# Kernel optimization log

Measured on AMD Instinct MI355X. Metric: run time of the kernel, lower is better.

Reference implementation:

```python
import jax, jax.numpy as jnp
import numpy as np

B, N, T, S = 32, 102400, 64, 1600
PI = float(np.pi)
EPS = 1e-12  # numerical guard inside sqrt for cdist (diagonal is exactly 0)


def _cdist(a, b):
    # a: (..., P, 3), b: (..., Q, 3) -> (..., P, Q) euclidean distances
    sq = jnp.sum((a[..., :, None, :] - b[..., None, :, :]) ** 2, axis=-1)
    return jnp.sqrt(sq + EPS)


def _rigid_t(alpha, trans, sz, center):
    # alpha, trans: (B, T, 3). Returns XYZ (B,T,3,3), translation (B,T,3).
    c, s = jnp.cos(alpha), jnp.sin(alpha)
    z = jnp.zeros_like(c[..., 0]); o = jnp.ones_like(c[..., 0])
    X = jnp.stack([c[..., 0], -s[..., 0], z, s[..., 0], c[..., 0], z, z, z, o], -1).reshape(*alpha.shape[:2], 3, 3)
    Y = jnp.stack([c[..., 1], z, s[..., 1], z, o, z, -s[..., 1], z, c[..., 1]], -1).reshape(*alpha.shape[:2], 3, 3)
    Z = jnp.stack([o, z, z, z, c[..., 2], -s[..., 2], z, s[..., 2], c[..., 2]], -1).reshape(*alpha.shape[:2], 3, 3)
    XYZ = jnp.einsum('btij,btjk,btkl->btil', X, Y, Z)
    eye = jnp.eye(3, dtype=alpha.dtype)
    Tt = trans * sz[None, None, :] + jnp.einsum('m,btmk->btk', center, eye[None, None] - XYZ)
    return XYZ, Tt


def setup_inputs():
    key = jax.random.key(0)
    ks = jax.random.split(key, 6)
    x = jax.random.normal(ks[0], (B, 6, N), jnp.float32)
    w1 = jax.random.normal(ks[1], (3 * N, 32), jnp.float32) * 0.005
    b1 = jnp.zeros((32,), jnp.float32)
    w2 = jax.random.normal(ks[2], (32, 6 * T), jnp.float32) * 0.05
    b2 = jnp.zeros((6 * T,), jnp.float32)
    A = jax.random.normal(ks[3], (6, N), jnp.float32)
    mask = jax.random.uniform(ks[4], (T, T), jnp.float32)
    sz = jnp.array([128.0, 128.0, 64.0], jnp.float32)
    tess = jnp.arange(N, dtype=jnp.int32).reshape(T, S)  # equal-size partition
    return {'x': x, 'w1': w1, 'b1': b1, 'w2': w2, 'b2': b2, 'A': A, 'mask': mask, 'sz': sz, 'tess': tess}


def reference(x, w1, b1, w2, b2, A, mask, sz, tess):
    center = sz / 2.0
    # localization MLP on flattened xyz coords: (B, 3N) -> (B, T, 6)
    xflat = x[:, :3, :].reshape(B, 3 * N)
    h = jax.nn.relu(xflat @ w1 + b1)
    z_l = jnp.tanh(h @ w2 + b2).reshape(B, T, 6)
    # NOTE: original code uses z_l[:, :, 3:] for BOTH angles and translation
    r_, t_ = _rigid_t(PI * z_l[:, :, 3:], z_l[:, :, 3:], sz, center)
    x3 = x[:, :3, :]
    xg = x3[:, :, tess]  # gather: (B, 3, T, S)
    # out[b,j,p,n] = sum_k r_[b,p,k,j] * xg[b,k,p,n]  (matches einsum 'bkt,bkn->btn')
    rot = jnp.einsum('bpkj,bkpn->bjpn', r_, xg) + t_.transpose(0, 2, 1)[:, :, :, None]
    # scatter back into full point cloud (tess partitions N)
    X3 = jnp.zeros_like(x3).at[:, :, tess.reshape(-1)].set(rot.reshape(B, 3, N))
    X_t = jnp.concatenate([X3, x[:, 3:, :]], axis=1)  # colors pass through identity
    # regularizer on per-piece centroids
    pts_1 = A[:3][:, tess].mean(axis=2).T                 # (T, 3)
    pts_2 = X3[:, :, tess].mean(axis=3).transpose(0, 2, 1)  # (B, T, 3)
    diff = _cdist(pts_1, pts_1)[None] - _cdist(pts_2, pts_2)
    reg = jnp.sum((mask[None] * diff) ** 2, axis=(1, 2))  # (B,)
    return X_t, reg
```

## Files before the change

kernel.cpp:

```cpp
#include <hip/hip_runtime.h>
#include <hip/hip_bf16.h>
#include <math.h>

#define BB 32
#define NN 102400
#define TT 64
#define SS 1600
#define K3N (3 * NN)
#define KC 256
#define G1 400
#define NCHUNK (K3N / KC)
#define PI_F 3.14159265358979323846f

__global__ __launch_bounds__(256) void k1_gemm(const float* __restrict__ x,
                                               const float* __restrict__ w1,
                                               float* __restrict__ h_part) {
    __shared__ float xs[32 * 260];
    __shared__ float ws1[KC * 32];
    const int tid = threadIdx.x;
    const int b = tid >> 3, cq = tid & 7;
    float a0 = 0.f, a1 = 0.f, a2 = 0.f, a3 = 0.f;

    for (int chunk = blockIdx.x; chunk < NCHUNK; chunk += G1) {
        const int k0 = chunk * KC;
        for (int i = tid; i < 32 * 64; i += 256) {
            const int bb = i >> 6, k4 = i & 63;
            const float4 v = *(const float4*)(x + (size_t)bb * 6 * NN + k0 + k4 * 4);
            *(float4*)(xs + bb * 260 + k4 * 4) = v;
        }
        for (int i = tid; i < (KC * 32) / 4; i += 256) {
            *(float4*)(ws1 + i * 4) = *(const float4*)(w1 + (size_t)k0 * 32 + i * 4);
        }
        __syncthreads();
        const float* xrow = xs + b * 260;
        #pragma unroll 8
        for (int k4 = 0; k4 < 64; ++k4) {
            const float4 xv = *(const float4*)(xrow + k4 * 4);
            #pragma unroll
            for (int j = 0; j < 4; ++j) {
                const float xj = j == 0 ? xv.x : (j == 1 ? xv.y : (j == 2 ? xv.z : xv.w));
                const float4 wv = *(const float4*)(ws1 + (k4 * 4 + j) * 32 + cq * 4);
                a0 = fmaf(xj, wv.x, a0);
                a1 = fmaf(xj, wv.y, a1);
                a2 = fmaf(xj, wv.z, a2);
                a3 = fmaf(xj, wv.w, a3);
            }
        }
        __syncthreads();
    }
    float4 r; r.x = a0; r.y = a1; r.z = a2; r.w = a3;
    *(float4*)(h_part + (size_t)blockIdx.x * 1024 + tid * 4) = r;
}

__global__ void k2a_reduce(const float* __restrict__ h_part, const float* __restrict__ b1,
                           float* __restrict__ h) {
    const int i = blockIdx.x * blockDim.x + threadIdx.x;
    float s = 0.f;
    for (int j = 0; j < G1; ++j) s += h_part[(size_t)j * 1024 + i];
    s += b1[i & 31];
    h[i] = fmaxf(s, 0.f);
}

__global__ void k2b_rigid(const float* __restrict__ h, const float* __restrict__ w2,
                          const float* __restrict__ b2, const float* __restrict__ sz,
                          float* __restrict__ RT) {
    const int g = blockIdx.x * blockDim.x + threadIdx.x;
    if (g >= BB * TT) return;
    const int b = g / TT, t = g % TT;
    const float* hb = h + b * 32;
    float z[3];
    #pragma unroll
    for (int j = 0; j < 3; ++j) {
        const int col = 6 * t + 3 + j;
        float s = b2[col];
        #pragma unroll 8
        for (int c = 0; c < 32; ++c) s = fmaf(hb[c], w2[c * 384 + col], s);
        z[j] = tanhf(s);
    }
    float c0, s0, c1, s1, c2, s2;
    sincosf(PI_F * z[0], &s0, &c0);
    sincosf(PI_F * z[1], &s1, &c1);
    sincosf(PI_F * z[2], &s2, &c2);
    const float R00 = c0 * c1;
    const float R01 = -s0 * c2 + c0 * s1 * s2;
    const float R02 = s0 * s2 + c0 * s1 * c2;
    const float R10 = s0 * c1;
    const float R11 = c0 * c2 + s0 * s1 * s2;
    const float R12 = -c0 * s2 + s0 * s1 * c2;
    const float R20 = -s1;
    const float R21 = c1 * s2;
    const float R22 = c1 * c2;
    const float szx = sz[0], szy = sz[1], szz = sz[2];
    const float cx = 0.5f * szx, cy = 0.5f * szy, cz = 0.5f * szz;
    const float T0 = z[0] * szx + cx - (cx * R00 + cy * R10 + cz * R20);
    const float T1 = z[1] * szy + cy - (cx * R01 + cy * R11 + cz * R21);
    const float T2 = z[2] * szz + cz - (cx * R02 + cy * R12 + cz * R22);
    float* o = RT + g * 12;
    o[0] = R00; o[1] = R10; o[2] = R20; o[3]  = T0;
    o[4] = R01; o[5] = R11; o[6] = R21; o[7]  = T1;
    o[8] = R02; o[9] = R12; o[10] = R22; o[11] = T2;
}

__global__ __launch_bounds__(256) void k3_transform(const float* __restrict__ x,
                                                    const int* __restrict__ tess,
                                                    const float* __restrict__ RT,
                                                    float* __restrict__ out,
                                                    float* __restrict__ pts2) {
    const int blk = blockIdx.x;
    const int b = blk / TT, t = blk % TT;
    const float* p = RT + blk * 12;
    const float M00 = p[0], M01 = p[1], M02 = p[2], T0 = p[3];
    const float M10 = p[4], M11 = p[5], M12 = p[6], T1 = p[7];
    const float M20 = p[8], M21 = p[9], M22 = p[10], T2 = p[11];
    const float* xb = x + (size_t)b * 6 * NN;
    float* ob = out + (size_t)b * 6 * NN;
    const int* tr = tess + t * SS;
    float s0 = 0.f, s1 = 0.f, s2 = 0.f;
    for (int s = threadIdx.x; s < SS; s += 256) {
        const int idx = tr[s];
        const float x0 = xb[idx], x1 = xb[NN + idx], x2 = xb[2 * NN + idx];
        const float y0 = fmaf(M00, x0, fmaf(M01, x1, fmaf(M02, x2, T0)));
        const float y1 = fmaf(M10, x0, fmaf(M11, x1, fmaf(M12, x2, T1)));
        const float y2 = fmaf(M20, x0, fmaf(M21, x1, fmaf(M22, x2, T2)));
        ob[idx] = y0; ob[NN + idx] = y1; ob[2 * NN + idx] = y2;
        s0 += y0; s1 += y1; s2 += y2;
        const int n = t * SS + s;
        ob[3 * NN + n] = xb[3 * NN + n];
        ob[4 * NN + n] = xb[4 * NN + n];
        ob[5 * NN + n] = xb[5 * NN + n];
    }
    #pragma unroll
    for (int o = 32; o > 0; o >>= 1) {
        s0 += __shfl_down(s0, o, 64);
        s1 += __shfl_down(s1, o, 64);
        s2 += __shfl_down(s2, o, 64);
    }
    __shared__ float red[4 * 3];
    const int lane = threadIdx.x & 63, wv = threadIdx.x >> 6;
    if (lane == 0) { red[wv * 3] = s0; red[wv * 3 + 1] = s1; red[wv * 3 + 2] = s2; }
    __syncthreads();
    if (threadIdx.x < 3) {
        const float s = red[threadIdx.x] + red[3 + threadIdx.x] + red[6 + threadIdx.x] + red[9 + threadIdx.x];
        pts2[blk * 3 + threadIdx.x] = s * (1.0f / SS);
    }
}

__global__ __launch_bounds__(256) void k4_pts1(const float* __restrict__ A,
                                               const int* __restrict__ tess,
                                               float* __restrict__ pts1) {
    const int t = blockIdx.x;
    const int* tr = tess + t * SS;
    float s0 = 0.f, s1 = 0.f, s2 = 0.f;
    for (int s = threadIdx.x; s < SS; s += 256) {
        const int idx = tr[s];
        s0 += A[idx]; s1 += A[NN + idx]; s2 += A[2 * NN + idx];
    }
    #pragma unroll
    for (int o = 32; o > 0; o >>= 1) {
        s0 += __shfl_down(s0, o, 64);
        s1 += __shfl_down(s1, o, 64);
        s2 += __shfl_down(s2, o, 64);
    }
    __shared__ float red[4 * 3];
    const int lane = threadIdx.x & 63, wv = threadIdx.x >> 6;
    if (lane == 0) { red[wv * 3] = s0; red[wv * 3 + 1] = s1; red[wv * 3 + 2] = s2; }
    __syncthreads();
    if (threadIdx.x < 3) {
        const float s = red[threadIdx.x] + red[3 + threadIdx.x] + red[6 + threadIdx.x] + red[9 + threadIdx.x];
        pts1[t * 3 + threadIdx.x] = s * (1.0f / SS);
    }
}

__global__ __launch_bounds__(256) void k5_reg(const float* __restrict__ pts1,
                                              const float* __restrict__ pts2,
                                              const float* __restrict__ mask,
                                              float* __restrict__ out) {
    const int b = blockIdx.x;
    __shared__ float p1[TT * 3], p2[TT * 3];
    for (int i = threadIdx.x; i < TT * 3; i += 256) {
        p1[i] = pts1[i];
        p2[i] = pts2[b * TT * 3 + i];
    }
    __syncthreads();
    float acc = 0.f;
    for (int pr = threadIdx.x; pr < TT * TT; pr += 256) {
        const int t = pr >> 6, u = pr & 63;
        float dx = p1[t * 3] - p1[u * 3];
        float dy = p1[t * 3 + 1] - p1[u * 3 + 1];
        float dz = p1[t * 3 + 2] - p1[u * 3 + 2];
        const float d1 = sqrtf(dx * dx + dy * dy + dz * dz + 1e-12f);
        dx = p2[t * 3] - p2[u * 3];
        dy = p2[t * 3 + 1] - p2[u * 3 + 1];
        dz = p2[t * 3 + 2] - p2[u * 3 + 2];
        const float d2 = sqrtf(dx * dx + dy * dy + dz * dz + 1e-12f);
        const float d = mask[pr] * (d1 - d2);
        acc = fmaf(d, d, acc);
    }
    #pragma unroll
    for (int o = 32; o > 0; o >>= 1) acc += __shfl_down(acc, o, 64);
    __shared__ float red[4];
    const int lane = threadIdx.x & 63, wv = threadIdx.x >> 6;
    if (lane == 0) red[wv] = acc;
    __syncthreads();
    if (threadIdx.x == 0) {
        out[(size_t)BB * 6 * NN + b] = red[0] + red[1] + red[2] + red[3];
    }
}

extern "C" void kernel_launch(void* const* d_in, const int* in_sizes, int n_in,
                              void* d_out, int out_size, void* d_ws, size_t ws_size,
                              hipStream_t stream) {
    const float* x    = (const float*)d_in[0];
    const float* w1   = (const float*)d_in[1];
    const float* b1   = (const float*)d_in[2];
    const float* w2   = (const float*)d_in[3];
    const float* b2   = (const float*)d_in[4];
    const float* A    = (const float*)d_in[5];
    const float* mask = (const float*)d_in[6];
    const float* sz   = (const float*)d_in[7];
    const int*   tess = (const int*)d_in[8];
    float* out = (float*)d_out;
    float* ws  = (float*)d_ws;

    float* h_part = ws;
    float* h      = h_part + G1 * 1024;
    float* RT     = h + 1024;
    float* pts2   = RT + BB * TT * 12;
    float* pts1   = pts2 + BB * TT * 3;

    k1_gemm<<<G1, 256, 0, stream>>>(x, w1, h_part);
    k2a_reduce<<<4, 256, 0, stream>>>(h_part, b1, h);
    k2b_rigid<<<(BB * TT + 255) / 256, 256, 0, stream>>>(h, w2, b2, sz, RT);
    k3_transform<<<BB * TT, 256, 0, stream>>>(x, tess, RT, out, pts2);
    k4_pts1<<<TT, 256, 0, stream>>>(A, tess, pts1);
    k5_reg<<<BB, 256, 0, stream>>>(pts1, pts2, mask, out);
}
```

Baseline: 84.69 us.

## Fuse reduce, rigid and pts1 kernels; retile GEMM chunks; vectorize color copy

Merges the partial-sum reduction, the rigid-transform computation and the pts1 centroid kernel into one launch that splits its blocks by role, removing two launches and the intermediate h buffer. The split-K GEMM now uses smaller K chunks (128) spread over more blocks (512) to raise occupancy, and the color passthrough copy becomes a separate float4 vectorized loop. The reduction now runs on 32 blocks and covers more partials per output, which could lengthen that stage.

```diff
diff --git a/kernel.cpp b/kernel.cpp
--- a/kernel.cpp
+++ b/kernel.cpp
@@ -7,15 +7,16 @@
 #define TT 64
 #define SS 1600
 #define K3N (3 * NN)
-#define KC 256
-#define G1 400
+#define KC 128
+#define G1 512
 #define NCHUNK (K3N / KC)
+#define XPAD 132
 #define PI_F 3.14159265358979323846f
 
 __global__ __launch_bounds__(256) void k1_gemm(const float* __restrict__ x,
                                                const float* __restrict__ w1,
                                                float* __restrict__ h_part) {
-    __shared__ float xs[32 * 260];
+    __shared__ float xs[32 * XPAD];
     __shared__ float ws1[KC * 32];
     const int tid = threadIdx.x;
     const int b = tid >> 3, cq = tid & 7;
@@ -23,18 +24,18 @@
 
     for (int chunk = blockIdx.x; chunk < NCHUNK; chunk += G1) {
         const int k0 = chunk * KC;
-        for (int i = tid; i < 32 * 64; i += 256) {
-            const int bb = i >> 6, k4 = i & 63;
+        for (int i = tid; i < 32 * 32; i += 256) {
+            const int bb = i >> 5, k4 = i & 31;
             const float4 v = *(const float4*)(x + (size_t)bb * 6 * NN + k0 + k4 * 4);
-            *(float4*)(xs + bb * 260 + k4 * 4) = v;
+            *(float4*)(xs + bb * XPAD + k4 * 4) = v;
         }
         for (int i = tid; i < (KC * 32) / 4; i += 256) {
             *(float4*)(ws1 + i * 4) = *(const float4*)(w1 + (size_t)k0 * 32 + i * 4);
         }
         __syncthreads();
-        const float* xrow = xs + b * 260;
+        const float* xrow = xs + b * XPAD;
         #pragma unroll 8
-        for (int k4 = 0; k4 < 64; ++k4) {
+        for (int k4 = 0; k4 < KC / 4; ++k4) {
             const float4 xv = *(const float4*)(xrow + k4 * 4);
             #pragma unroll
             for (int j = 0; j < 4; ++j) {
@@ -52,53 +53,89 @@
     *(float4*)(h_part + (size_t)blockIdx.x * 1024 + tid * 4) = r;
 }
 
-__global__ void k2a_reduce(const float* __restrict__ h_part, const float* __restrict__ b1,
-                           float* __restrict__ h) {
-    const int i = blockIdx.x * blockDim.x + threadIdx.x;
-    float s = 0.f;
-    for (int j = 0; j < G1; ++j) s += h_part[(size_t)j * 1024 + i];
-    s += b1[i & 31];
-    h[i] = fmaxf(s, 0.f);
-}
-
-__global__ void k2b_rigid(const float* __restrict__ h, const float* __restrict__ w2,
-                          const float* __restrict__ b2, const float* __restrict__ sz,
-                          float* __restrict__ RT) {
-    const int g = blockIdx.x * blockDim.x + threadIdx.x;
-    if (g >= BB * TT) return;
-    const int b = g / TT, t = g % TT;
-    const float* hb = h + b * 32;
-    float z[3];
-    #pragma unroll
-    for (int j = 0; j < 3; ++j) {
-        const int col = 6 * t + 3 + j;
-        float s = b2[col];
-        #pragma unroll 8
-        for (int c = 0; c < 32; ++c) s = fmaf(hb[c], w2[c * 384 + col], s);
-        z[j] = tanhf(s);
-    }
-    float c0, s0, c1, s1, c2, s2;
-    sincosf(PI_F * z[0], &s0, &c0);
-    sincosf(PI_F * z[1], &s1, &c1);
-    sincosf(PI_F * z[2], &s2, &c2);
-    const float R00 = c0 * c1;
-    const float R01 = -s0 * c2 + c0 * s1 * s2;
-    const float R02 = s0 * s2 + c0 * s1 * c2;
-    const float R10 = s0 * c1;
-    const float R11 = c0 * c2 + s0 * s1 * s2;
-    const float R12 = -c0 * s2 + s0 * s1 * c2;
-    const float R20 = -s1;
-    const float R21 = c1 * s2;
-    const float R22 = c1 * c2;
-    const float szx = sz[0], szy = sz[1], szz = sz[2];
-    const float cx = 0.5f * szx, cy = 0.5f * szy, cz = 0.5f * szz;
-    const float T0 = z[0] * szx + cx - (cx * R00 + cy * R10 + cz * R20);
-    const float T1 = z[1] * szy + cy - (cx * R01 + cy * R11 + cz * R21);
-    const float T2 = z[2] * szz + cz - (cx * R02 + cy * R12 + cz * R22);
-    float* o = RT + g * 12;
-    o[0] = R00; o[1] = R10; o[2] = R20; o[3]  = T0;
-    o[4] = R01; o[5] = R11; o[6] = R21; o[7]  = T1;
-    o[8] = R02; o[9] = R12; o[10] = R22; o[11] = T2;
+__global__ __launch_bounds__(256) void kb_fused(const float* __restrict__ h_part,
+                                                const float* __restrict__ b1,
+                                                const float* __restrict__ w2,
+                                                const float* __restrict__ b2,
+                                                const float* __restrict__ sz,
+                                                const float* __restrict__ A,
+                                                const int* __restrict__ tess,
+                                                float* __restrict__ RT,
+                                                float* __restrict__ pts1) {
+    const int blk = blockIdx.x;
+    if (blk < BB) {
+        const int bb = blk;
+        __shared__ float part[8][32];
+        __shared__ float hsh[32];
+        const int c = threadIdx.x & 31, g = threadIdx.x >> 5;
+        float s = 0.f;
+        for (int j = g; j < G1; j += 8) s += h_part[(size_t)j * 1024 + bb * 32 + c];
+        part[g][c] = s;
+        __syncthreads();
+        if (threadIdx.x < 32) {
+            float acc = 0.f;
+            #pragma unroll
+            for (int g2 = 0; g2 < 8; ++g2) acc += part[g2][threadIdx.x];
+            hsh[threadIdx.x] = fmaxf(acc + b1[threadIdx.x], 0.f);
+        }
+        __syncthreads();
+        const int t = threadIdx.x;
+        if (t < TT) {
+            float z[3];
+            #pragma unroll
+            for (int j = 0; j < 3; ++j) {
+                const int col = 6 * t + 3 + j;
+                float s2 = b2[col];
+                #pragma unroll 8
+                for (int cc = 0; cc < 32; ++cc) s2 = fmaf(hsh[cc], w2[cc * 384 + col], s2);
+                z[j] = tanhf(s2);
+            }
+            float c0, s0, c1, s1, c2, s2v;
+            sincosf(PI_F * z[0], &s0, &c0);
+            sincosf(PI_F * z[1], &s1, &c1);
+            sincosf(PI_F * z[2], &s2v, &c2);
+            const float R00 = c0 * c1;
+            const float R01 = -s0 * c2 + c0 * s1 * s2v;
+            const float R02 = s0 * s2v + c0 * s1 * c2;
+            const float R10 = s0 * c1;
+            const float R11 = c0 * c2 + s0 * s1 * s2v;
+            const float R12 = -c0 * s2v + s0 * s1 * c2;
+            const float R20 = -s1;
+            const float R21 = c1 * s2v;
+            const float R22 = c1 * c2;
+            const float szx = sz[0], szy = sz[1], szz = sz[2];
+            const float cx = 0.5f * szx, cy = 0.5f * szy, cz = 0.5f * szz;
+            const float T0 = z[0] * szx + cx - (cx * R00 + cy * R10 + cz * R20);
+            const float T1 = z[1] * szy + cy - (cx * R01 + cy * R11 + cz * R21);
+            const float T2 = z[2] * szz + cz - (cx * R02 + cy * R12 + cz * R22);
+            float* o = RT + (bb * TT + t) * 12;
+            o[0] = R00; o[1] = R10; o[2]  = R20; o[3]  = T0;
+            o[4] = R01; o[5] = R11; o[6]  = R21; o[7]  = T1;
+            o[8] = R02; o[9] = R12; o[10] = R22; o[11] = T2;
+        }
+    } else {
+        const int t = blk - BB;
+        const int* tr = tess + t * SS;
+        float s0 = 0.f, s1 = 0.f, s2 = 0.f;
+        for (int s = threadIdx.x; s < SS; s += 256) {
+            const int idx = tr[s];
+            s0 += A[idx]; s1 += A[NN + idx]; s2 += A[2 * NN + idx];
+        }
+        #pragma unroll
+        for (int o = 32; o > 0; o >>= 1) {
+            s0 += __shfl_down(s0, o, 64);
+            s1 += __shfl_down(s1, o, 64);
+            s2 += __shfl_down(s2, o, 64);
+        }
+        __shared__ float red[4 * 3];
+        const int lane = threadIdx.x & 63, wv = threadIdx.x >> 6;
+        if (lane == 0) { red[wv * 3] = s0; red[wv * 3 + 1] = s1; red[wv * 3 + 2] = s2; }
+        __syncthreads();
+        if (threadIdx.x < 3) {
+            const float s = red[threadIdx.x] + red[3 + threadIdx.x] + red[6 + threadIdx.x] + red[9 + threadIdx.x];
+            pts1[t * 3 + threadIdx.x] = s * (1.0f / SS);
+        }
+    }
 }
 
 __global__ __launch_bounds__(256) void k3_transform(const float* __restrict__ x,
@@ -124,10 +161,12 @@
         const float y2 = fmaf(M20, x0, fmaf(M21, x1, fmaf(M22, x2, T2)));
         ob[idx] = y0; ob[NN + idx] = y1; ob[2 * NN + idx] = y2;
         s0 += y0; s1 += y1; s2 += y2;
-        const int n = t * SS + s;
-        ob[3 * NN + n] = xb[3 * NN + n];
-        ob[4 * NN + n] = xb[4 * NN + n];
-        ob[5 * NN + n] = xb[5 * NN + n];
+    }
+    const int n0 = t * SS;
+    for (int i = threadIdx.x; i < 1200; i += 256) {
+        const int ch = i / 400, r = i - ch * 400;
+        const size_t off = (size_t)(3 + ch) * NN + n0 + r * 4;
+        *(float4*)(ob + off) = *(const float4*)(xb + off);
     }
     #pragma unroll
     for (int o = 32; o > 0; o >>= 1) {
@@ -142,32 +181,6 @@
     if (threadIdx.x < 3) {
         const float s = red[threadIdx.x] + red[3 + threadIdx.x] + red[6 + threadIdx.x] + red[9 + threadIdx.x];
         pts2[blk * 3 + threadIdx.x] = s * (1.0f / SS);
-    }
-}
-
-__global__ __launch_bounds__(256) void k4_pts1(const float* __restrict__ A,
-                                               const int* __restrict__ tess,
-                                               float* __restrict__ pts1) {
-    const int t = blockIdx.x;
-    const int* tr = tess + t * SS;
-    float s0 = 0.f, s1 = 0.f, s2 = 0.f;
-    for (int s = threadIdx.x; s < SS; s += 256) {
-        const int idx = tr[s];
-        s0 += A[idx]; s1 += A[NN + idx]; s2 += A[2 * NN + idx];
-    }
-    #pragma unroll
-    for (int o = 32; o > 0; o >>= 1) {
-        s0 += __shfl_down(s0, o, 64);
-        s1 += __shfl_down(s1, o, 64);
-        s2 += __shfl_down(s2, o, 64);
-    }
-    __shared__ float red[4 * 3];
-    const int lane = threadIdx.x & 63, wv = threadIdx.x >> 6;
-    if (lane == 0) { red[wv * 3] = s0; red[wv * 3 + 1] = s1; red[wv * 3 + 2] = s2; }
-    __syncthreads();
-    if (threadIdx.x < 3) {
-        const float s = red[threadIdx.x] + red[3 + threadIdx.x] + red[6 + threadIdx.x] + red[9 + threadIdx.x];
-        pts1[t * 3 + threadIdx.x] = s * (1.0f / SS);
     }
 }
 
@@ -223,15 +236,12 @@
     float* ws  = (float*)d_ws;
 
     float* h_part = ws;
-    float* h      = h_part + G1 * 1024;
-    float* RT     = h + 1024;
+    float* RT     = h_part + G1 * 1024;
     float* pts2   = RT + BB * TT * 12;
     float* pts1   = pts2 + BB * TT * 3;
 
     k1_gemm<<<G1, 256, 0, stream>>>(x, w1, h_part);
-    k2a_reduce<<<4, 256, 0, stream>>>(h_part, b1, h);
-    k2b_rigid<<<(BB * TT + 255) / 256, 256, 0, stream>>>(h, w2, b2, sz, RT);
+    kb_fused<<<BB + TT, 256, 0, stream>>>(h_part, b1, w2, b2, sz, A, tess, RT, pts1);
     k3_transform<<<BB * TT, 256, 0, stream>>>(x, tess, RT, out, pts2);
-    k4_pts1<<<TT, 256, 0, stream>>>(A, tess, pts1);
     k5_reg<<<BB, 256, 0, stream>>>(pts1, pts2, mask, out);
 }
```

Result: slower. 90.07 us (+6.4%).
